# Kernel optimization log

Measured on AMD Instinct MI355X. Metric: run time of the kernel, lower is better.

## Reference

```python
import jax, jax.numpy as jnp
import numpy as np

OVERALL_W = (0.4, 0.4, 0.1, 0.1)


def nn_distance(pc1, pc2):
    # pc1: (B,N,3), pc2: (B,M,3) -> squared NN distance each way.
    # ||a-b||^2 = ||a||^2 + ||b||^2 - 2 a.b ; compute via batched GEMM.
    n1 = jnp.sum(pc1 * pc1, axis=-1)  # (B,N)
    n2 = jnp.sum(pc2 * pc2, axis=-1)  # (B,M)
    cross = jnp.einsum('bnd,bmd->bnm', pc1, pc2)  # (B,N,M)
    d = n1[:, :, None] + n2[:, None, :] - 2.0 * cross  # (B,N,M)
    dist1 = jnp.min(d, axis=2)  # (B,N)
    dist2 = jnp.min(d, axis=1)  # (B,M)
    return dist1, dist2


def setup_inputs() -> dict:
    key = jax.random.key(0)
    ks = jax.random.split(key, 7)
    bs, n_pts, num_hypo, cap_len = 16, 4096, 64, 77
    return {
        'shape_query': jax.random.normal(ks[0], (bs, n_pts, 3), dtype=jnp.float32),
        'logits': jax.random.normal(ks[1], (bs, num_hypo), dtype=jnp.float32),
        'pair_caption': jax.random.randint(ks[2], (bs, 2, cap_len), 0, 30000),
        'caption_embed': jax.random.randint(ks[3], (bs, 3, cap_len), 0, 30000),
        'sdf_pred': jax.random.normal(ks[4], (bs, 1, n_pts), dtype=jnp.float32),
        'prior': jax.random.normal(ks[5], (bs, 1024, 3), dtype=jnp.float32),
        'model': jax.random.normal(ks[6], (bs, 4096, 3), dtype=jnp.float32),
    }


def reference(shape_query, logits, pair_caption, caption_embed, sdf_pred, prior, model):
    log_prob = jax.nn.log_softmax(logits, axis=-1)
    pose_loss = -jnp.mean(log_prob[:, 0])
    reconstructed = jnp.concatenate([shape_query, prior], axis=1)  # (B, N+1024, 3)
    dist1, dist2 = nn_distance(reconstructed, model)
    shape_loss = jnp.mean(dist1) + jnp.mean(dist2)
    sdf_loss = shape_loss
    caption_loss = shape_loss
    loss = (OVERALL_W[0] * pose_loss + OVERALL_W[1] * shape_loss
            + OVERALL_W[2] * sdf_loss + OVERALL_W[3] * caption_loss)
    return (loss, pose_loss, shape_loss, sdf_loss, caption_loss)
```

## Files before the change

kernel.cpp:

```cpp
#include <hip/hip_runtime.h>
#include <math.h>

#define BATCH   16
#define NQ      4096
#define NPRIOR  1024
#define NREC    5120
#define NMODEL  4096
#define NHYP    64

#define NQD1    (BATCH*NREC)
#define NQD2    (BATCH*NMODEL)

#define TILE_COLS 512
#define P1_ROWBLKS (NREC/128)
#define P2_ROWBLKS (NMODEL/128)
#define P1_BLOCKS (BATCH*P1_ROWBLKS)
#define P2_BLOCKS (BATCH*P2_ROWBLKS)
#define GBLOCKS   (P1_BLOCKS + P2_BLOCKS)
#define P1_NTILES (NMODEL/TILE_COLS)
#define P2_NTILES (NREC/TILE_COLS)

#define WS_WORDS (NQD1 + NQD2 + 1)
#define WS_BYTES ((size_t)WS_WORDS*4)
#define RED_BLOCKS 128

typedef _Float16 half8  __attribute__((ext_vector_type(8)));
typedef float    f32x16 __attribute__((ext_vector_type(16)));

__device__ __forceinline__ float min3f(float a, float b, float c) {
    float d;
    asm("v_min3_f32 %0, %1, %2, %3" : "=v"(d) : "v"(a), "v"(b), "v"(c));
    return d;
}

__device__ __forceinline__ void packQ2(float x, float y, float z,
                                       half8& hi, half8& lo) {
    float n = fmaf(z, z, fmaf(y, y, x * x));
    float mx = -2.0f * x, my = -2.0f * y, mz = -2.0f * z;
    _Float16 xh = (_Float16)mx, yh = (_Float16)my, zh = (_Float16)mz;
    _Float16 nh = (_Float16)n;
    _Float16 xl = (_Float16)(mx - (float)xh);
    _Float16 yl = (_Float16)(my - (float)yh);
    _Float16 zl = (_Float16)(mz - (float)zh);
    _Float16 nl = (_Float16)(n - (float)nh);
    hi[0] = xh; hi[1] = yh; hi[2] = zh; hi[3] = nh;
    hi[4] = (_Float16)1.0f; hi[5] = xh; hi[6] = yh; hi[7] = zh;
    lo[0] = xl; lo[1] = yl; lo[2] = zl; lo[3] = nl;
    lo[4] = (_Float16)1.0f; lo[5] = (_Float16)0.0f;
    lo[6] = (_Float16)0.0f; lo[7] = (_Float16)0.0f;
}
__device__ __forceinline__ void packR2(float x, float y, float z,
                                       half8& hi, half8& lo) {
    float n = fmaf(z, z, fmaf(y, y, x * x));
    _Float16 xh = (_Float16)x, yh = (_Float16)y, zh = (_Float16)z;
    _Float16 nh = (_Float16)n;
    _Float16 xl = (_Float16)(x - (float)xh);
    _Float16 yl = (_Float16)(y - (float)yh);
    _Float16 zl = (_Float16)(z - (float)zh);
    _Float16 nl = (_Float16)(n - (float)nh);
    hi[0] = xh; hi[1] = yh; hi[2] = zh; hi[3] = (_Float16)1.0f;
    hi[4] = nh; hi[5] = xl; hi[6] = yl; hi[7] = zl;
    lo[0] = xh; lo[1] = yh; lo[2] = zh; lo[3] = (_Float16)1.0f;
    lo[4] = nl; lo[5] = (_Float16)0.0f;
    lo[6] = (_Float16)0.0f; lo[7] = (_Float16)0.0f;
}

__device__ __forceinline__ const float* rec_ptr(
    const float* __restrict__ shape_query, const float* __restrict__ prior,
    int b, int g) {
    return (g < NQ) ? shape_query + ((size_t)b * NQ + g) * 3
                    : prior + ((size_t)b * NPRIOR + (g - NQ)) * 3;
}

__global__ __launch_bounds__(256) void chamfer_hp(
    const float* __restrict__ shape_query,
    const float* __restrict__ prior,
    const float* __restrict__ model,
    float* __restrict__ ws, float* __restrict__ out) {
    __shared__ half8 Alds2[2 * 128];
    __shared__ half8 Blds2[2 * TILE_COLS];

    const int blk = blockIdx.x;
    if (blk == 0 && threadIdx.x == 0) {
        out[2] = 0.0f; out[3] = 0.0f;
        ((unsigned*)ws)[WS_WORDS - 1] = 0u;
    }

    const int t    = threadIdx.x;
    const int wave = t >> 6;
    const int lane = t & 63;
    const int l31  = lane & 31;
    const int kh   = lane >> 5;

    int b, rowbase, ntiles;
    float* rowplane;
    const bool pass1 = (blk < P1_BLOCKS);
    if (pass1) {
        b = blk / P1_ROWBLKS;
        rowbase = (blk % P1_ROWBLKS) * 128;
        ntiles = P1_NTILES;
        rowplane = ws + (size_t)b * NREC + rowbase;
    } else {
        int j = blk - P1_BLOCKS;
        b = j / P2_ROWBLKS;
        rowbase = (j % P2_ROWBLKS) * 128;
        ntiles = P2_NTILES;
        rowplane = ws + NQD1 + (size_t)b * NMODEL + rowbase;
    }

    if (t < 128) {
        const float* p = pass1
            ? rec_ptr(shape_query, prior, b, rowbase + t)
            : model + ((size_t)b * NMODEL + rowbase + t) * 3;
        half8 hi, lo;
        packQ2(p[0], p[1], p[2], hi, lo);
        Alds2[t] = hi; Alds2[128 + t] = lo;
    }

    float rmn[16];
#pragma unroll
    for (int r = 0; r < 16; ++r) rmn[r] = 3.0e38f;

    f32x16 cz;
#pragma unroll
    for (int i = 0; i < 16; ++i) cz[i] = 0.0f;

    const int boff = kh * TILE_COLS;
    half8 af;

    for (int tile = 0; tile < ntiles; ++tile) {
        if (tile) __syncthreads();
        const int colbase = tile * TILE_COLS;
#pragma unroll
        for (int c = t; c < TILE_COLS; c += 256) {
            const float* p = pass1
                ? model + ((size_t)b * NMODEL + colbase + c) * 3
                : rec_ptr(shape_query, prior, b, colbase + c);
            half8 hi, lo;
            packR2(p[0], p[1], p[2], hi, lo);
            Blds2[c] = hi; Blds2[TILE_COLS + c] = lo;
        }
        __syncthreads();

        af = Alds2[kh * 128 + wave * 32 + l31];

        half8 bfa = Blds2[boff + l31];
        half8 bfb = Blds2[boff + 32 + l31];
#pragma unroll 2
        for (int it = 0; it < TILE_COLS / 64; ++it) {
            const int nxt = (it == TILE_COLS / 64 - 1) ? 0 : (it + 1) * 64;
            half8 bfa_n = Blds2[boff + nxt + l31];
            half8 bfb_n = Blds2[boff + nxt + 32 + l31];
            f32x16 da = __builtin_amdgcn_mfma_f32_32x32x16_f16(af, bfa, cz, 0, 0, 0);
            f32x16 db = __builtin_amdgcn_mfma_f32_32x32x16_f16(af, bfb, cz, 0, 0, 0);
#pragma unroll
            for (int r = 0; r < 16; ++r) rmn[r] = min3f(rmn[r], da[r], db[r]);
            bfa = bfa_n; bfb = bfb_n;
        }
    }

#pragma unroll
    for (int r = 0; r < 16; ++r) {
        float v = rmn[r];
        v = fminf(v, __shfl_xor(v, 1, 64));
        v = fminf(v, __shfl_xor(v, 2, 64));
        v = fminf(v, __shfl_xor(v, 4, 64));
        v = fminf(v, __shfl_xor(v, 8, 64));
        v = fminf(v, __shfl_xor(v, 16, 64));
        if (l31 == 0) {
            int row = wave * 32 + (r & 3) + 8 * (r >> 2) + 4 * kh;
            rowplane[row] = v;
        }
    }
}

__global__ __launch_bounds__(256) void reduce_finalize2(
    const float* __restrict__ ws, const float* __restrict__ logits,
    float* __restrict__ out, unsigned int* __restrict__ counter) {
    float s1 = 0.0f, s2 = 0.0f;
    const int tot = NQD1 + NQD2;
    for (int i = blockIdx.x * 256 + threadIdx.x; i < tot;
         i += RED_BLOCKS * 256) {
        float v = ws[i];
        if (i < NQD1) s1 += v; else s2 += v;
    }
#pragma unroll
    for (int off = 32; off > 0; off >>= 1) {
        s1 += __shfl_xor(s1, off, 64);
        s2 += __shfl_xor(s2, off, 64);
    }
    __shared__ float a1[4], a2[4];
    __shared__ int last;
    int w = threadIdx.x >> 6;
    if ((threadIdx.x & 63) == 0) { a1[w] = s1; a2[w] = s2; }
    __syncthreads();
    if (threadIdx.x == 0) {
        atomicAdd(&out[2], a1[0] + a1[1] + a1[2] + a1[3]);
        atomicAdd(&out[3], a2[0] + a2[1] + a2[2] + a2[3]);
        __threadfence();
        unsigned done = atomicAdd(counter, 1u);
        last = (done == RED_BLOCKS - 1) ? 1 : 0;
    }
    __syncthreads();
    if (last && threadIdx.x < 64) {
        const int lane = threadIdx.x;
        float pose_part = 0.0f;
        if (lane < BATCH) {
            const float* L = logits + lane * NHYP;
            float mx = L[0];
#pragma unroll 8
            for (int j = 1; j < NHYP; ++j) mx = fmaxf(mx, L[j]);
            float s = 0.0f;
#pragma unroll 8
            for (int j = 0; j < NHYP; ++j) s += expf(L[j] - mx);
            pose_part = L[0] - (mx + logf(s));
        }
#pragma unroll
        for (int off = 8; off > 0; off >>= 1)
            pose_part += __shfl_xor(pose_part, off, 64);
        if (lane == 0) {
            float sum1 = atomicAdd(&out[2], 0.0f);
            float sum2 = atomicAdd(&out[3], 0.0f);
            float shape_loss = sum1 / (float)NQD1 + sum2 / (float)NQD2;
            float pose_loss = -pose_part / (float)BATCH;
            out[0] = 0.4f * pose_loss + 0.6f * shape_loss;
            out[1] = pose_loss;
            out[2] = shape_loss;
            out[3] = shape_loss;
            out[4] = shape_loss;
        }
    }
}


__global__ void init_out(float* out) {
    if (threadIdx.x == 0) { out[2] = 0.0f; out[3] = 0.0f; }
}

__device__ __forceinline__ void scan_refs(const float* __restrict__ r, int cnt,
                                          float px, float py, float pz,
                                          float& minv) {
    for (int m = 0; m < cnt; m += 8) {
#pragma unroll
        for (int u = 0; u < 8; ++u) {
            float mx = r[(m + u) * 3 + 0];
            float my = r[(m + u) * 3 + 1];
            float mz = r[(m + u) * 3 + 2];
            float dx = px - mx, dy = py - my, dz = pz - mz;
            float d = fmaf(dz, dz, fmaf(dy, dy, dx * dx));
            minv = fminf(minv, d);
        }
    }
}

__global__ __launch_bounds__(64) void chamfer_sum(
    const float* __restrict__ qa, int na_, const float* __restrict__ qb, int nb_,
    const float* __restrict__ ra, int ma, const float* __restrict__ rb, int mb,
    float* __restrict__ accum) {
    const int b = blockIdx.y;
    const int n = blockIdx.x * 64 + threadIdx.x;
    float px, py, pz;
    if (n < na_) {
        const float* p = qa + ((size_t)b * na_ + n) * 3;
        px = p[0]; py = p[1]; pz = p[2];
    } else {
        const float* p = qb + ((size_t)b * nb_ + (n - na_)) * 3;
        px = p[0]; py = p[1]; pz = p[2];
    }
    float minv = 3.0e38f;
    scan_refs(ra + (size_t)b * ma * 3, ma, px, py, pz, minv);
    if (mb > 0) scan_refs(rb + (size_t)b * mb * 3, mb, px, py, pz, minv);
    float s = minv;
#pragma unroll
    for (int off = 32; off > 0; off >>= 1) s += __shfl_xor(s, off, 64);
    if (threadIdx.x == 0) atomicAdd(accum, s);
}

__global__ __launch_bounds__(64) void finalize_kernel(
    const float* __restrict__ logits, float* __restrict__ out) {
    const int lane = threadIdx.x;
    float pose_part = 0.0f;
    if (lane < BATCH) {
        const float* L = logits + lane * NHYP;
        float mx = L[0];
#pragma unroll 8
        for (int j = 1; j < NHYP; ++j) mx = fmaxf(mx, L[j]);
        float s = 0.0f;
#pragma unroll 8
        for (int j = 0; j < NHYP; ++j) s += expf(L[j] - mx);
        pose_part = L[0] - (mx + logf(s));
    }
#pragma unroll
    for (int off = 8; off > 0; off >>= 1) pose_part += __shfl_xor(pose_part, off, 64);
    if (lane == 0) {
        float shape_loss = out[2] / (float)NQD1 + out[3] / (float)NQD2;
        float pose_loss = -pose_part / (float)BATCH;
        out[0] = 0.4f * pose_loss + 0.6f * shape_loss;
        out[1] = pose_loss;
        out[2] = shape_loss;
        out[3] = shape_loss;
        out[4] = shape_loss;
    }
}

extern "C" void kernel_launch(void* const* d_in, const int* in_sizes, int n_in,
                              void* d_out, int out_size, void* d_ws, size_t ws_size,
                              hipStream_t stream) {
    const float* shape_query = (const float*)d_in[0];
    const float* logits      = (const float*)d_in[1];
    const float* prior       = (const float*)d_in[5];
    const float* model       = (const float*)d_in[6];
    float* out = (float*)d_out;

    if (ws_size >= WS_BYTES) {
        float* ws = (float*)d_ws;
        unsigned int* counter = (unsigned int*)ws + (WS_WORDS - 1);
        hipLaunchKernelGGL(chamfer_hp, dim3(GBLOCKS), dim3(256), 0, stream,
                           shape_query, prior, model, ws, out);
        hipLaunchKernelGGL(reduce_finalize2, dim3(RED_BLOCKS), dim3(256), 0,
                           stream, ws, logits, out, counter);
    } else {
        hipLaunchKernelGGL(init_out, dim3(1), dim3(64), 0, stream, out);
        hipLaunchKernelGGL(chamfer_sum,
                           dim3(NREC / 64, BATCH), dim3(64), 0, stream,
                           shape_query, NQ, prior, NPRIOR,
                           model, NMODEL, (const float*)nullptr, 0, out + 2);
        hipLaunchKernelGGL(chamfer_sum,
                           dim3(NMODEL / 64, BATCH), dim3(64), 0, stream,
                           model, NMODEL, (const float*)nullptr, 0,
                           shape_query, NQ, prior, NPRIOR, out + 3);
        hipLaunchKernelGGL(finalize_kernel, dim3(1), dim3(64), 0, stream,
                           logits, out);
    }
}
```

Baseline: 60.35 us.

## Split column range across two blocks and prefetch next tile into registers

```diff
diff --git a/kernel.cpp b/kernel.cpp
--- a/kernel.cpp
+++ b/kernel.cpp
@@ -14,13 +14,15 @@
 #define TILE_COLS 512
 #define P1_ROWBLKS (NREC/128)
 #define P2_ROWBLKS (NMODEL/128)
-#define P1_BLOCKS (BATCH*P1_ROWBLKS)
-#define P2_BLOCKS (BATCH*P2_ROWBLKS)
+#define P1_CHUNKS 2
+#define P2_CHUNKS 2
+#define P1_NTILES (NMODEL/TILE_COLS/P1_CHUNKS)
+#define P2_NTILES (NREC/TILE_COLS/P2_CHUNKS)
+#define P1_BLOCKS (BATCH*P1_ROWBLKS*P1_CHUNKS)
+#define P2_BLOCKS (BATCH*P2_ROWBLKS*P2_CHUNKS)
 #define GBLOCKS   (P1_BLOCKS + P2_BLOCKS)
-#define P1_NTILES (NMODEL/TILE_COLS)
-#define P2_NTILES (NREC/TILE_COLS)
-
-#define WS_WORDS (NQD1 + NQD2 + 1)
+
+#define WS_WORDS (P1_CHUNKS*NQD1 + P2_CHUNKS*NQD2 + 1)
 #define WS_BYTES ((size_t)WS_WORDS*4)
 #define RED_BLOCKS 128
 
@@ -92,20 +94,27 @@
     const int l31  = lane & 31;
     const int kh   = lane >> 5;
 
-    int b, rowbase, ntiles;
+    int b, rowbase, colbase0, ntiles;
     float* rowplane;
     const bool pass1 = (blk < P1_BLOCKS);
     if (pass1) {
-        b = blk / P1_ROWBLKS;
-        rowbase = (blk % P1_ROWBLKS) * 128;
+        b = blk / (P1_ROWBLKS * P1_CHUNKS);
+        int rem = blk % (P1_ROWBLKS * P1_CHUNKS);
+        int rb = rem / P1_CHUNKS, ck = rem % P1_CHUNKS;
+        rowbase = rb * 128;
+        colbase0 = ck * (P1_NTILES * TILE_COLS);
         ntiles = P1_NTILES;
-        rowplane = ws + (size_t)b * NREC + rowbase;
+        rowplane = ws + (size_t)ck * NQD1 + b * NREC + rowbase;
     } else {
         int j = blk - P1_BLOCKS;
-        b = j / P2_ROWBLKS;
-        rowbase = (j % P2_ROWBLKS) * 128;
+        b = j / (P2_ROWBLKS * P2_CHUNKS);
+        int rem = j % (P2_ROWBLKS * P2_CHUNKS);
+        int rb = rem / P2_CHUNKS, ck = rem % P2_CHUNKS;
+        rowbase = rb * 128;
+        colbase0 = ck * (P2_NTILES * TILE_COLS);
         ntiles = P2_NTILES;
-        rowplane = ws + NQD1 + (size_t)b * NMODEL + rowbase;
+        rowplane = ws + (size_t)P1_CHUNKS * NQD1 + (size_t)ck * NQD2
+                   + b * NMODEL + rowbase;
     }
 
     if (t < 128) {
@@ -117,6 +126,20 @@
         Alds2[t] = hi; Alds2[128 + t] = lo;
     }
 
+    {
+        const float* p0 = pass1
+            ? model + ((size_t)b * NMODEL + colbase0 + t) * 3
+            : rec_ptr(shape_query, prior, b, colbase0 + t);
+        const float* p1 = pass1
+            ? model + ((size_t)b * NMODEL + colbase0 + 256 + t) * 3
+            : rec_ptr(shape_query, prior, b, colbase0 + 256 + t);
+        half8 hi, lo;
+        packR2(p0[0], p0[1], p0[2], hi, lo);
+        Blds2[t] = hi; Blds2[TILE_COLS + t] = lo;
+        packR2(p1[0], p1[1], p1[2], hi, lo);
+        Blds2[256 + t] = hi; Blds2[TILE_COLS + 256 + t] = lo;
+    }
+
     float rmn[16];
 #pragma unroll
     for (int r = 0; r < 16; ++r) rmn[r] = 3.0e38f;
@@ -126,24 +149,25 @@
     for (int i = 0; i < 16; ++i) cz[i] = 0.0f;
 
     const int boff = kh * TILE_COLS;
-    half8 af;
+
+    __syncthreads();
 
     for (int tile = 0; tile < ntiles; ++tile) {
-        if (tile) __syncthreads();
-        const int colbase = tile * TILE_COLS;
-#pragma unroll
-        for (int c = t; c < TILE_COLS; c += 256) {
-            const float* p = pass1
-                ? model + ((size_t)b * NMODEL + colbase + c) * 3
-                : rec_ptr(shape_query, prior, b, colbase + c);
-            half8 hi, lo;
-            packR2(p[0], p[1], p[2], hi, lo);
-            Blds2[c] = hi; Blds2[TILE_COLS + c] = lo;
-        }
-        __syncthreads();
-
-        af = Alds2[kh * 128 + wave * 32 + l31];
-
+        float nx0, ny0, nz0, nx1, ny1, nz1;
+        const bool more = (tile + 1 < ntiles);
+        if (more) {
+            const int cb = colbase0 + (tile + 1) * TILE_COLS;
+            const float* p0 = pass1
+                ? model + ((size_t)b * NMODEL + cb + t) * 3
+                : rec_ptr(shape_query, prior, b, cb + t);
+            const float* p1 = pass1
+                ? model + ((size_t)b * NMODEL + cb + 256 + t) * 3
+                : rec_ptr(shape_query, prior, b, cb + 256 + t);
+            nx0 = p0[0]; ny0 = p0[1]; nz0 = p0[2];
+            nx1 = p1[0]; ny1 = p1[1]; nz1 = p1[2];
+        }
+
+        half8 af = Alds2[kh * 128 + wave * 32 + l31];
         half8 bfa = Blds2[boff + l31];
         half8 bfb = Blds2[boff + 32 + l31];
 #pragma unroll 2
@@ -156,6 +180,16 @@
 #pragma unroll
             for (int r = 0; r < 16; ++r) rmn[r] = min3f(rmn[r], da[r], db[r]);
             bfa = bfa_n; bfb = bfb_n;
+        }
+
+        __syncthreads();
+        if (more) {
+            half8 hi, lo;
+            packR2(nx0, ny0, nz0, hi, lo);
+            Blds2[t] = hi; Blds2[TILE_COLS + t] = lo;
+            packR2(nx1, ny1, nz1, hi, lo);
+            Blds2[256 + t] = hi; Blds2[TILE_COLS + 256 + t] = lo;
+            __syncthreads();
         }
     }
 
@@ -177,12 +211,18 @@
 __global__ __launch_bounds__(256) void reduce_finalize2(
     const float* __restrict__ ws, const float* __restrict__ logits,
     float* __restrict__ out, unsigned int* __restrict__ counter) {
+    const float* p1 = ws;
+    const float* p2 = ws + (size_t)P1_CHUNKS * NQD1;
     float s1 = 0.0f, s2 = 0.0f;
     const int tot = NQD1 + NQD2;
     for (int i = blockIdx.x * 256 + threadIdx.x; i < tot;
          i += RED_BLOCKS * 256) {
-        float v = ws[i];
-        if (i < NQD1) s1 += v; else s2 += v;
+        if (i < NQD1) {
+            s1 += fminf(p1[i], p1[NQD1 + i]);
+        } else {
+            int j = i - NQD1;
+            s2 += fminf(p2[j], p2[NQD2 + j]);
+        }
     }
 #pragma unroll
     for (int off = 32; off > 0; off >>= 1) {
```

Result: faster. 57.81 us (-4.2%).
